# Performance work log

Measured on AMD Instinct MI355X. Metric: run time of the kernel, lower is better.

## Reference

```python
import jax, jax.numpy as jnp
import numpy as np

N_NODES = 100_000
N_EDGES = 3_200_000
WEIGHT_LIMIT = 5000.0
RIDGE = 1e-7


def _polynomial_basis(diff):
    # diff: [E, 2] -> [E, 5] basis (x, y, x*y, x^2, y^2)
    x = diff[:, 0]
    y = diff[:, 1]
    return jnp.stack([x, y, x * y, x * x, y * y], axis=-1)


def setup_inputs() -> dict:
    key = jax.random.key(0)
    k1, k2, k3 = jax.random.split(key, 3)
    pos = jax.random.normal(k1, (N_NODES, 2), dtype=jnp.float32)
    row = jax.random.randint(k2, (N_EDGES,), 0, N_NODES, dtype=jnp.int64)
    col = jax.random.randint(k3, (N_EDGES,), 0, N_NODES, dtype=jnp.int64)
    edge_index = jnp.stack([row, col], axis=0)
    return {"pos": pos, "edge_index": edge_index}


def reference(pos, edge_index):
    # With a dense random graph, 2-hop extension adds no edges, so the
    # augmented edge_index equals the original edge_index.
    row = edge_index[0]
    col = edge_index[1]
    n = pos.shape[0]

    # Edge displacement (detached in the original module).
    diff = jax.lax.stop_gradient(pos[col] - pos[row])  # [E, 2]
    H = _polynomial_basis(diff).astype(jnp.float32)    # [E, 5]

    # Per-edge outer products, scatter-accumulated per source node.
    M_edge = H[:, :, None] * H[:, None, :]                          # [E, 5, 5]
    M_node = jax.ops.segment_sum(M_edge, row, num_segments=n)      # [N, 5, 5]
    M_node = M_node + RIDGE * jnp.eye(5, dtype=jnp.float32)

    # Laplacian RHS: [0, 0, 0, 2, 2] per node (coefficients of x^2, y^2).
    L = jnp.zeros((n, 5), dtype=jnp.float32).at[:, 3:].set(2.0)

    # C = M^{-1} L (per-node 5x5 solve).
    C = jnp.linalg.solve(M_node, L[..., None])[..., 0]              # [N, 5]

    # Per-edge Laplacian weights.
    weights = jnp.sum(C[row] * H, axis=1)                           # [E]
    return jnp.clip(weights, -WEIGHT_LIMIT, WEIGHT_LIMIT)
```

## Files before the change

### kernel.cpp

```cpp
#include <hip/hip_runtime.h>
#include <math.h>

constexpr float WLIM = 5000.0f;
constexpr double RIDGE = 1e-7;

#define G 256
#define MAXNB 1024
#define BN 128
#define CAP 5120
#define EBUF_CAP 12544

__global__ __launch_bounds__(1024) void k_sort(const int* __restrict__ row,
                                               const int* __restrict__ col,
                                               int* __restrict__ table,
                                               unsigned int* __restrict__ sorted,
                                               int nE, int CE, int NB) {
    __shared__ int h[MAXNB];
    __shared__ int wt[16];
    __shared__ unsigned int ebuf[EBUF_CAP];
    const int g = blockIdx.x, tid = threadIdx.x;
    const int lane = tid & 63, wid = tid >> 6;
    const int s = g * CE;
    const int e_end = min(s + CE, nE);
    const int cnt = e_end - s;
    const bool vec = ((CE & 3) == 0);

    for (int i = tid; i < MAXNB; i += 1024) h[i] = 0;
    __syncthreads();
    if (vec) {
        const int4* r4p = (const int4*)(row + s);
        int nv = cnt >> 2;
        for (int i = tid; i < nv; i += 1024) {
            int4 r4 = r4p[i];
            atomicAdd(&h[r4.x >> 7], 1);
            atomicAdd(&h[r4.y >> 7], 1);
            atomicAdd(&h[r4.z >> 7], 1);
            atomicAdd(&h[r4.w >> 7], 1);
        }
        for (int i = (nv << 2) + tid; i < cnt; i += 1024)
            atomicAdd(&h[row[s + i] >> 7], 1);
    } else {
        for (int i = s + tid; i < e_end; i += 1024)
            atomicAdd(&h[row[i] >> 7], 1);
    }
    __syncthreads();
    int v = h[tid];
    int x = v;
    #pragma unroll
    for (int d = 1; d < 64; d <<= 1) {
        int u = __shfl_up(x, d);
        if (lane >= d) x += u;
    }
    if (lane == 63) wt[wid] = x;
    __syncthreads();
    if (tid < 16) {
        int w = wt[tid];
        int xx = w;
        #pragma unroll
        for (int d = 1; d < 16; d <<= 1) {
            int u = __shfl_up(xx, d);
            if (tid >= d) xx += u;
        }
        wt[tid] = xx - w;
    }
    __syncthreads();
    int excl = (x - v) + wt[wid];
    if (tid < NB) {
        table[(size_t)tid * G + g] = excl;
        h[tid] = excl;
    }
    if (tid == 0) table[(size_t)NB * G + g] = cnt;
    __syncthreads();
    if (vec) {
        const int4* r4p = (const int4*)(row + s);
        const int4* c4p = (const int4*)(col + s);
        int nv = cnt >> 2;
        for (int i = tid; i < nv; i += 1024) {
            int4 r4 = r4p[i];
            int4 c4 = c4p[i];
            int p;
            p = atomicAdd(&h[r4.x >> 7], 1); ebuf[p] = ((unsigned)(r4.x & 127) << 17) | (unsigned)c4.x;
            p = atomicAdd(&h[r4.y >> 7], 1); ebuf[p] = ((unsigned)(r4.y & 127) << 17) | (unsigned)c4.y;
            p = atomicAdd(&h[r4.z >> 7], 1); ebuf[p] = ((unsigned)(r4.z & 127) << 17) | (unsigned)c4.z;
            p = atomicAdd(&h[r4.w >> 7], 1); ebuf[p] = ((unsigned)(r4.w & 127) << 17) | (unsigned)c4.w;
        }
        for (int i = (nv << 2) + tid; i < cnt; i += 1024) {
            int r = row[s + i], c = col[s + i];
            int p = atomicAdd(&h[r >> 7], 1);
            ebuf[p] = ((unsigned)(r & 127) << 17) | (unsigned)c;
        }
    } else {
        for (int i = s + tid; i < e_end; i += 1024) {
            int r = row[i], c = col[i];
            int p = atomicAdd(&h[r >> 7], 1);
            ebuf[p] = ((unsigned)(r & 127) << 17) | (unsigned)c;
        }
    }
    __syncthreads();
    if (vec) {
        uint4* dst = (uint4*)(sorted + s);
        const uint4* src = (const uint4*)ebuf;
        int nv = cnt >> 2;
        for (int i = tid; i < nv; i += 1024) dst[i] = src[i];
        for (int i = (nv << 2) + tid; i < cnt; i += 1024) sorted[s + i] = ebuf[i];
    } else {
        for (int i = tid; i < cnt; i += 1024) sorted[s + i] = ebuf[i];
    }
}

__global__ __launch_bounds__(256) void k_node3(const float2* __restrict__ pos,
                                               const unsigned int* __restrict__ sorted,
                                               const int* __restrict__ table,
                                               float* __restrict__ rec,
                                               int nN, int CE, int NB) {
    __shared__ unsigned int ebuf[CAP];
    __shared__ int cnt[BN];
    __shared__ int off[BN + 1];
    __shared__ int cur[BN];
    __shared__ int goff0[G], glen[G];
    __shared__ int wt2[2];
    const int b = blockIdx.x, tid = threadIdx.x;

    int off0 = table[(size_t)b * G + tid];
    int off1 = table[(size_t)(b + 1) * G + tid];
    int len = off1 - off0;
    goff0[tid] = off0; glen[tid] = len;
    if (tid < BN) cnt[tid] = 0;
    __syncthreads();

    const int gbase = tid * CE + off0;
    for (int j = 0; j < len; ++j)
        atomicAdd(&cnt[sorted[gbase + j] >> 17], 1);
    __syncthreads();
    int sv = 0, sx = 0;
    if (tid < BN) {
        sv = cnt[tid];
        sx = sv;
        #pragma unroll
        for (int d = 1; d < 64; d <<= 1) {
            int u = __shfl_up(sx, d);
            if ((tid & 63) >= d) sx += u;
        }
        if ((tid & 63) == 63) wt2[tid >> 6] = sx;
    }
    __syncthreads();
    if (tid < BN) {
        int incl = sx + ((tid >> 6) ? wt2[0] : 0);
        off[tid] = incl - sv;
        cur[tid] = incl - sv;
        if (tid == BN - 1) off[BN] = incl;
    }
    __syncthreads();
    const int total = off[BN];

    const bool fits = (total <= CAP);
    if (fits) {
        for (int j = 0; j < len; ++j) {
            unsigned v = sorted[gbase + j];
            int p = atomicAdd(&cur[(int)(v >> 17)], 1);
            ebuf[p] = v & 0x1FFFFu;
        }
    }
    __syncthreads();

    const int node = tid >> 1;
    const int half = tid & 1;
    const int n = (b << 7) + node;
    float m[15];
    #pragma unroll
    for (int i = 0; i < 15; ++i) m[i] = 0.0f;
    float2 pr = make_float2(0.f, 0.f);
    if (n < nN) {
        pr = pos[n];
        if (fits) {
            int j0 = off[node], j1 = off[node + 1];
            for (int j = j0 + half; j < j1; j += 2) {
                float2 pc = pos[ebuf[j]];
                float x = pc.x - pr.x;
                float y = pc.y - pr.y;
                float xy = x * y, xx = x * x, yy = y * y;
                m[0]  += x * x;   m[1]  += x * y;   m[2]  += x * xy;  m[3]  += x * xx;  m[4]  += x * yy;
                m[5]  += y * y;   m[6]  += y * xy;  m[7]  += y * xx;  m[8]  += y * yy;
                m[9]  += xy * xy; m[10] += xy * xx; m[11] += xy * yy;
                m[12] += xx * xx; m[13] += xx * yy;
                m[14] += yy * yy;
            }
        } else {
            for (int g2 = half; g2 < G; g2 += 2) {
                int base2 = g2 * CE + goff0[g2];
                for (int j = 0; j < glen[g2]; ++j) {
                    unsigned v = sorted[base2 + j];
                    if ((int)(v >> 17) == node) {
                        float2 pc = pos[v & 0x1FFFFu];
                        float x = pc.x - pr.x;
                        float y = pc.y - pr.y;
                        float xy = x * y, xx = x * x, yy = y * y;
                        m[0]  += x * x;   m[1]  += x * y;   m[2]  += x * xy;  m[3]  += x * xx;  m[4]  += x * yy;
                        m[5]  += y * y;   m[6]  += y * xy;  m[7]  += y * xx;  m[8]  += y * yy;
                        m[9]  += xy * xy; m[10] += xy * xx; m[11] += xy * yy;
                        m[12] += xx * xx; m[13] += xx * yy;
                        m[14] += yy * yy;
                    }
                }
            }
        }
    }
    #pragma unroll
    for (int i = 0; i < 15; ++i) m[i] += __shfl_xor(m[i], 1);

    if (half == 0 && n < nN) {
        double A[5][5];
        {
            int idx = 0;
            #pragma unroll
            for (int i = 0; i < 5; ++i) {
                #pragma unroll
                for (int j = i; j < 5; ++j) {
                    double vv = (double)m[idx++];
                    A[i][j] = vv;
                    A[j][i] = vv;
                }
            }
        }
        #pragma unroll
        for (int i = 0; i < 5; ++i) A[i][i] += RIDGE;

        #pragma unroll
        for (int k = 0; k < 5; ++k) {
            double d = A[k][k];
            d = sqrt(fmax(d, 1e-300));
            A[k][k] = d;
            double inv = 1.0 / d;
            #pragma unroll
            for (int i = k + 1; i < 5; ++i) A[i][k] *= inv;
            #pragma unroll
            for (int j = k + 1; j < 5; ++j) {
                #pragma unroll
                for (int i = j; i < 5; ++i) A[i][j] -= A[i][k] * A[j][k];
            }
        }
        double bb[5] = {0.0, 0.0, 0.0, 2.0, 2.0};
        double y[5];
        #pragma unroll
        for (int i = 0; i < 5; ++i) {
            double sv2 = bb[i];
            #pragma unroll
            for (int k = 0; k < 5; ++k) {
                if (k < i) sv2 -= A[i][k] * y[k];
            }
            y[i] = sv2 / A[i][i];
        }
        double xs[5];
        #pragma unroll
        for (int ii = 4; ii >= 0; --ii) {
            double sv2 = y[ii];
            #pragma unroll
            for (int k = 0; k < 5; ++k) {
                if (k > ii) sv2 -= A[k][ii] * xs[k];
            }
            xs[ii] = sv2 / A[ii][ii];
        }
        float4* rb = (float4*)(rec + (size_t)n * 8);
        rb[0] = make_float4((float)xs[0], (float)xs[1], (float)xs[2], (float)xs[3]);
        rb[1] = make_float4((float)xs[4], pr.x, pr.y, 0.0f);
    }
}

__global__ __launch_bounds__(256) void k_weights(const float2* __restrict__ pos,
                                                 const int* __restrict__ row,
                                                 const int* __restrict__ col,
                                                 const float* __restrict__ rec,
                                                 float* __restrict__ out,
                                                 int nE) {
    int e = blockIdx.x * blockDim.x + threadIdx.x;
    if (e >= nE) return;
    int r = __builtin_nontemporal_load(row + e);
    int c = __builtin_nontemporal_load(col + e);
    const float4* rb = (const float4*)(rec + (size_t)r * 8);
    float4 q0 = rb[0];
    float4 q1 = rb[1];
    float2 pc = pos[c];
    float x = pc.x - q1.y;
    float y = pc.y - q1.z;
    float w = q0.x * x + q0.y * y + q0.z * (x * y) + q0.w * (x * x) + q1.x * (y * y);
    w = fminf(fmaxf(w, -WLIM), WLIM);
    __builtin_nontemporal_store(w, out + e);
}

extern "C" void kernel_launch(void* const* d_in, const int* in_sizes, int n_in,
                              void* d_out, int out_size, void* d_ws, size_t ws_size,
                              hipStream_t stream) {
    const float2* pos = (const float2*)d_in[0];
    const int* ei = (const int*)d_in[1];
    const int nN = in_sizes[0] / 2;
    const int nE = in_sizes[1] / 2;
    const int* row = ei;
    const int* col = ei + nE;

    const int NB = (nN + BN - 1) >> 7;
    const int CE = (nE + G - 1) / G;

    int* table = (int*)d_ws;
    size_t roff = (((size_t)(NB + 1) * G) + 3) & ~(size_t)3;
    float* rec = (float*)((int*)d_ws + roff);

    unsigned int* sorted = (unsigned int*)d_out;
    float* out = (float*)d_out;

    k_sort<<<G, 1024, 0, stream>>>(row, col, table, sorted, nE, CE, NB);
    k_node3<<<NB, 256, 0, stream>>>(pos, sorted, table, rec, nN, CE, NB);
    k_weights<<<(nE + 255) / 256, 256, 0, stream>>>(pos, row, col, rec, out, nE);
}
```

Measured before the change: 85.12 us.

## Split edge bucketing into more smaller blocks and process two chunks per thread

The bucketing kernel now uses 512 blocks of 512 threads, each holding half the edge chunk in shared memory. Each thread now handles two histogram bins, and the chunk size is padded to a multiple of four so the vector path always applies. The node kernel reads two group chunks per thread, interleaved to expose more memory parallelism. The weights kernel moves to 1024-thread blocks. The intent is more parallelism and occupancy in the sort stage. The cost is a larger offset table and more serial work per thread in the node kernel.

```diff
diff --git a/kernel.cpp b/kernel.cpp
--- a/kernel.cpp
+++ b/kernel.cpp
@@ -4,47 +4,45 @@
 constexpr float WLIM = 5000.0f;
 constexpr double RIDGE = 1e-7;
 
-#define G 256
+#define G 512
+#define SBT 512
 #define MAXNB 1024
 #define BN 128
 #define CAP 5120
-#define EBUF_CAP 12544
-
-__global__ __launch_bounds__(1024) void k_sort(const int* __restrict__ row,
-                                               const int* __restrict__ col,
-                                               int* __restrict__ table,
-                                               unsigned int* __restrict__ sorted,
-                                               int nE, int CE, int NB) {
+#define EBUF_CAP 6272
+
+__global__ __launch_bounds__(SBT) void k_sort(const int* __restrict__ row,
+                                              const int* __restrict__ col,
+                                              int* __restrict__ table,
+                                              unsigned int* __restrict__ sorted,
+                                              int nE, int CE, int NB) {
     __shared__ int h[MAXNB];
-    __shared__ int wt[16];
+    __shared__ int wt[SBT / 64];
     __shared__ unsigned int ebuf[EBUF_CAP];
     const int g = blockIdx.x, tid = threadIdx.x;
     const int lane = tid & 63, wid = tid >> 6;
     const int s = g * CE;
     const int e_end = min(s + CE, nE);
-    const int cnt = e_end - s;
-    const bool vec = ((CE & 3) == 0);
-
-    for (int i = tid; i < MAXNB; i += 1024) h[i] = 0;
-    __syncthreads();
-    if (vec) {
+    const int cnt = max(0, e_end - s);
+
+    for (int i = tid; i < MAXNB; i += SBT) h[i] = 0;
+    __syncthreads();
+    {
         const int4* r4p = (const int4*)(row + s);
         int nv = cnt >> 2;
-        for (int i = tid; i < nv; i += 1024) {
+        for (int i = tid; i < nv; i += SBT) {
             int4 r4 = r4p[i];
             atomicAdd(&h[r4.x >> 7], 1);
             atomicAdd(&h[r4.y >> 7], 1);
             atomicAdd(&h[r4.z >> 7], 1);
             atomicAdd(&h[r4.w >> 7], 1);
         }
-        for (int i = (nv << 2) + tid; i < cnt; i += 1024)
+        for (int i = (nv << 2) + tid; i < cnt; i += SBT)
             atomicAdd(&h[row[s + i] >> 7], 1);
-    } else {
-        for (int i = s + tid; i < e_end; i += 1024)
-            atomicAdd(&h[row[i] >> 7], 1);
-    }
-    __syncthreads();
-    int v = h[tid];
+    }
+    __syncthreads();
+    int v0 = h[2 * tid], v1 = h[2 * tid + 1];
+    int v = v0 + v1;
     int x = v;
     #pragma unroll
     for (int d = 1; d < 64; d <<= 1) {
@@ -53,29 +51,30 @@
     }
     if (lane == 63) wt[wid] = x;
     __syncthreads();
-    if (tid < 16) {
+    if (tid < SBT / 64) {
         int w = wt[tid];
         int xx = w;
         #pragma unroll
-        for (int d = 1; d < 16; d <<= 1) {
+        for (int d = 1; d < SBT / 64; d <<= 1) {
             int u = __shfl_up(xx, d);
             if (tid >= d) xx += u;
         }
         wt[tid] = xx - w;
     }
     __syncthreads();
-    int excl = (x - v) + wt[wid];
-    if (tid < NB) {
-        table[(size_t)tid * G + g] = excl;
-        h[tid] = excl;
-    }
+    int base = (x - v) + wt[wid];
+    int e0 = base, e1 = base + v0;
+    if (2 * tid < NB)     table[(size_t)(2 * tid) * G + g] = e0;
+    if (2 * tid + 1 < NB) table[(size_t)(2 * tid + 1) * G + g] = e1;
     if (tid == 0) table[(size_t)NB * G + g] = cnt;
-    __syncthreads();
-    if (vec) {
+    h[2 * tid] = e0;
+    h[2 * tid + 1] = e1;
+    __syncthreads();
+    {
         const int4* r4p = (const int4*)(row + s);
         const int4* c4p = (const int4*)(col + s);
         int nv = cnt >> 2;
-        for (int i = tid; i < nv; i += 1024) {
+        for (int i = tid; i < nv; i += SBT) {
             int4 r4 = r4p[i];
             int4 c4 = c4p[i];
             int p;
@@ -84,27 +83,19 @@
             p = atomicAdd(&h[r4.z >> 7], 1); ebuf[p] = ((unsigned)(r4.z & 127) << 17) | (unsigned)c4.z;
             p = atomicAdd(&h[r4.w >> 7], 1); ebuf[p] = ((unsigned)(r4.w & 127) << 17) | (unsigned)c4.w;
         }
-        for (int i = (nv << 2) + tid; i < cnt; i += 1024) {
+        for (int i = (nv << 2) + tid; i < cnt; i += SBT) {
             int r = row[s + i], c = col[s + i];
             int p = atomicAdd(&h[r >> 7], 1);
             ebuf[p] = ((unsigned)(r & 127) << 17) | (unsigned)c;
         }
-    } else {
-        for (int i = s + tid; i < e_end; i += 1024) {
-            int r = row[i], c = col[i];
-            int p = atomicAdd(&h[r >> 7], 1);
-            ebuf[p] = ((unsigned)(r & 127) << 17) | (unsigned)c;
-        }
-    }
-    __syncthreads();
-    if (vec) {
+    }
+    __syncthreads();
+    {
         uint4* dst = (uint4*)(sorted + s);
         const uint4* src = (const uint4*)ebuf;
         int nv = cnt >> 2;
-        for (int i = tid; i < nv; i += 1024) dst[i] = src[i];
-        for (int i = (nv << 2) + tid; i < cnt; i += 1024) sorted[s + i] = ebuf[i];
-    } else {
-        for (int i = tid; i < cnt; i += 1024) sorted[s + i] = ebuf[i];
+        for (int i = tid; i < nv; i += SBT) dst[i] = src[i];
+        for (int i = (nv << 2) + tid; i < cnt; i += SBT) sorted[s + i] = ebuf[i];
     }
 }
 
@@ -120,17 +111,33 @@
     __shared__ int goff0[G], glen[G];
     __shared__ int wt2[2];
     const int b = blockIdx.x, tid = threadIdx.x;
-
-    int off0 = table[(size_t)b * G + tid];
-    int off1 = table[(size_t)(b + 1) * G + tid];
-    int len = off1 - off0;
-    goff0[tid] = off0; glen[tid] = len;
+    const int tB = tid + 256;
+
+    int offA0 = table[(size_t)b * G + tid];
+    int offA1 = table[(size_t)(b + 1) * G + tid];
+    int offB0 = table[(size_t)b * G + tB];
+    int offB1 = table[(size_t)(b + 1) * G + tB];
+    int lenA = offA1 - offA0;
+    int lenB = offB1 - offB0;
+    goff0[tid] = offA0; glen[tid] = lenA;
+    goff0[tB] = offB0;  glen[tB] = lenB;
     if (tid < BN) cnt[tid] = 0;
     __syncthreads();
 
-    const int gbase = tid * CE + off0;
-    for (int j = 0; j < len; ++j)
-        atomicAdd(&cnt[sorted[gbase + j] >> 17], 1);
+    const int gbaseA = tid * CE + offA0;
+    const int gbaseB = tB * CE + offB0;
+    {
+        int j = 0;
+        int lmin = min(lenA, lenB);
+        for (; j < lmin; ++j) {
+            unsigned va = sorted[gbaseA + j];
+            unsigned vb = sorted[gbaseB + j];
+            atomicAdd(&cnt[va >> 17], 1);
+            atomicAdd(&cnt[vb >> 17], 1);
+        }
+        for (; j < lenA; ++j) atomicAdd(&cnt[sorted[gbaseA + j] >> 17], 1);
+        for (; j < lenB; ++j) atomicAdd(&cnt[sorted[gbaseB + j] >> 17], 1);
+    }
     __syncthreads();
     int sv = 0, sx = 0;
     if (tid < BN) {
@@ -155,10 +162,25 @@
 
     const bool fits = (total <= CAP);
     if (fits) {
-        for (int j = 0; j < len; ++j) {
-            unsigned v = sorted[gbase + j];
-            int p = atomicAdd(&cur[(int)(v >> 17)], 1);
-            ebuf[p] = v & 0x1FFFFu;
+        int j = 0;
+        int lmin = min(lenA, lenB);
+        for (; j < lmin; ++j) {
+            unsigned va = sorted[gbaseA + j];
+            unsigned vb = sorted[gbaseB + j];
+            int pa = atomicAdd(&cur[(int)(va >> 17)], 1);
+            ebuf[pa] = va & 0x1FFFFu;
+            int pb = atomicAdd(&cur[(int)(vb >> 17)], 1);
+            ebuf[pb] = vb & 0x1FFFFu;
+        }
+        for (; j < lenA; ++j) {
+            unsigned va = sorted[gbaseA + j];
+            int pa = atomicAdd(&cur[(int)(va >> 17)], 1);
+            ebuf[pa] = va & 0x1FFFFu;
+        }
+        for (; j < lenB; ++j) {
+            unsigned vb = sorted[gbaseB + j];
+            int pb = atomicAdd(&cur[(int)(vb >> 17)], 1);
+            ebuf[pb] = vb & 0x1FFFFu;
         }
     }
     __syncthreads();
@@ -266,12 +288,12 @@
     }
 }
 
-__global__ __launch_bounds__(256) void k_weights(const float2* __restrict__ pos,
-                                                 const int* __restrict__ row,
-                                                 const int* __restrict__ col,
-                                                 const float* __restrict__ rec,
-                                                 float* __restrict__ out,
-                                                 int nE) {
+__global__ __launch_bounds__(1024) void k_weights(const float2* __restrict__ pos,
+                                                  const int* __restrict__ row,
+                                                  const int* __restrict__ col,
+                                                  const float* __restrict__ rec,
+                                                  float* __restrict__ out,
+                                                  int nE) {
     int e = blockIdx.x * blockDim.x + threadIdx.x;
     if (e >= nE) return;
     int r = __builtin_nontemporal_load(row + e);
@@ -298,7 +320,7 @@
     const int* col = ei + nE;
 
     const int NB = (nN + BN - 1) >> 7;
-    const int CE = (nE + G - 1) / G;
+    const int CE = (((nE + G - 1) / G) + 3) & ~3;
 
     int* table = (int*)d_ws;
     size_t roff = (((size_t)(NB + 1) * G) + 3) & ~(size_t)3;
@@ -307,7 +329,7 @@
     unsigned int* sorted = (unsigned int*)d_out;
     float* out = (float*)d_out;
 
-    k_sort<<<G, 1024, 0, stream>>>(row, col, table, sorted, nE, CE, NB);
+    k_sort<<<G, SBT, 0, stream>>>(row, col, table, sorted, nE, CE, NB);
     k_node3<<<NB, 256, 0, stream>>>(pos, sorted, table, rec, nN, CE, NB);
-    k_weights<<<(nE + 255) / 256, 256, 0, stream>>>(pos, row, col, rec, out, nE);
+    k_weights<<<(nE + 1023) / 1024, 1024, 0, stream>>>(pos, row, col, rec, out, nE);
 }
```

Result: slower. 114.4 us (+34.4%).

## Compute edge weights in sorted order inside node kernel, then unsort via posmap

Applied to the files above, without the earlier changes.

The separate per-edge weights kernel is removed. Each node block now keeps its solved coefficients in shared memory and computes weights for its bucket-sorted edges, writing them in place over the sorted buffer. The sort kernel also records a 16-bit local position for every edge. A new unsort kernel uses that position to put the weights back in original edge order. This avoids re-reading row/col and gathering per-node records from global memory, but adds posmap traffic, an extra full pass over the edges, and a per-thread serial loop with poorly coalesced accesses in the node kernel.

```diff
diff --git a/kernel.cpp b/kernel.cpp
--- a/kernel.cpp
+++ b/kernel.cpp
@@ -14,6 +14,7 @@
                                                const int* __restrict__ col,
                                                int* __restrict__ table,
                                                unsigned int* __restrict__ sorted,
+                                               unsigned short* __restrict__ posmap,
                                                int nE, int CE, int NB) {
     __shared__ int h[MAXNB];
     __shared__ int wt[16];
@@ -74,26 +75,30 @@
     if (vec) {
         const int4* r4p = (const int4*)(row + s);
         const int4* c4p = (const int4*)(col + s);
+        ushort4* pm4 = (ushort4*)(posmap + s);
         int nv = cnt >> 2;
         for (int i = tid; i < nv; i += 1024) {
             int4 r4 = r4p[i];
             int4 c4 = c4p[i];
-            int p;
-            p = atomicAdd(&h[r4.x >> 7], 1); ebuf[p] = ((unsigned)(r4.x & 127) << 17) | (unsigned)c4.x;
-            p = atomicAdd(&h[r4.y >> 7], 1); ebuf[p] = ((unsigned)(r4.y & 127) << 17) | (unsigned)c4.y;
-            p = atomicAdd(&h[r4.z >> 7], 1); ebuf[p] = ((unsigned)(r4.z & 127) << 17) | (unsigned)c4.z;
-            p = atomicAdd(&h[r4.w >> 7], 1); ebuf[p] = ((unsigned)(r4.w & 127) << 17) | (unsigned)c4.w;
+            int p0 = atomicAdd(&h[r4.x >> 7], 1); ebuf[p0] = ((unsigned)(r4.x & 127) << 17) | (unsigned)c4.x;
+            int p1 = atomicAdd(&h[r4.y >> 7], 1); ebuf[p1] = ((unsigned)(r4.y & 127) << 17) | (unsigned)c4.y;
+            int p2 = atomicAdd(&h[r4.z >> 7], 1); ebuf[p2] = ((unsigned)(r4.z & 127) << 17) | (unsigned)c4.z;
+            int p3 = atomicAdd(&h[r4.w >> 7], 1); ebuf[p3] = ((unsigned)(r4.w & 127) << 17) | (unsigned)c4.w;
+            pm4[i] = make_ushort4((unsigned short)p0, (unsigned short)p1,
+                                  (unsigned short)p2, (unsigned short)p3);
         }
         for (int i = (nv << 2) + tid; i < cnt; i += 1024) {
             int r = row[s + i], c = col[s + i];
             int p = atomicAdd(&h[r >> 7], 1);
             ebuf[p] = ((unsigned)(r & 127) << 17) | (unsigned)c;
+            posmap[s + i] = (unsigned short)p;
         }
     } else {
-        for (int i = s + tid; i < e_end; i += 1024) {
-            int r = row[i], c = col[i];
+        for (int i = tid; i < cnt; i += 1024) {
+            int r = row[s + i], c = col[s + i];
             int p = atomicAdd(&h[r >> 7], 1);
             ebuf[p] = ((unsigned)(r & 127) << 17) | (unsigned)c;
+            posmap[s + i] = (unsigned short)p;
         }
     }
     __syncthreads();
@@ -109,9 +114,8 @@
 }
 
 __global__ __launch_bounds__(256) void k_node3(const float2* __restrict__ pos,
-                                               const unsigned int* __restrict__ sorted,
+                                               unsigned int* __restrict__ sorted,
                                                const int* __restrict__ table,
-                                               float* __restrict__ rec,
                                                int nN, int CE, int NB) {
     __shared__ unsigned int ebuf[CAP];
     __shared__ int cnt[BN];
@@ -119,6 +123,7 @@
     __shared__ int cur[BN];
     __shared__ int goff0[G], glen[G];
     __shared__ int wt2[2];
+    __shared__ float crec[BN * 8];
     const int b = blockIdx.x, tid = threadIdx.x;
 
     int off0 = table[(size_t)b * G + tid];
@@ -260,31 +265,59 @@
             }
             xs[ii] = sv2 / A[ii][ii];
         }
-        float4* rb = (float4*)(rec + (size_t)n * 8);
-        rb[0] = make_float4((float)xs[0], (float)xs[1], (float)xs[2], (float)xs[3]);
-        rb[1] = make_float4((float)xs[4], pr.x, pr.y, 0.0f);
+        float* cb = &crec[node * 8];
+        #pragma unroll
+        for (int i = 0; i < 5; ++i) cb[i] = (float)xs[i];
+        cb[5] = pr.x;
+        cb[6] = pr.y;
+    }
+    __syncthreads();
+
+    float* wout = (float*)sorted;
+    for (int j = 0; j < len; ++j) {
+        unsigned v = sorted[gbase + j];
+        int lr = (int)(v >> 17);
+        int c = (int)(v & 0x1FFFFu);
+        const float* cb = &crec[lr * 8];
+        float2 pc = pos[c];
+        float x = pc.x - cb[5];
+        float y = pc.y - cb[6];
+        float w = cb[0] * x + cb[1] * y + cb[2] * (x * y) + cb[3] * (x * x) + cb[4] * (y * y);
+        w = fminf(fmaxf(w, -WLIM), WLIM);
+        wout[gbase + j] = w;
     }
 }
 
-__global__ __launch_bounds__(256) void k_weights(const float2* __restrict__ pos,
-                                                 const int* __restrict__ row,
-                                                 const int* __restrict__ col,
-                                                 const float* __restrict__ rec,
-                                                 float* __restrict__ out,
-                                                 int nE) {
-    int e = blockIdx.x * blockDim.x + threadIdx.x;
-    if (e >= nE) return;
-    int r = __builtin_nontemporal_load(row + e);
-    int c = __builtin_nontemporal_load(col + e);
-    const float4* rb = (const float4*)(rec + (size_t)r * 8);
-    float4 q0 = rb[0];
-    float4 q1 = rb[1];
-    float2 pc = pos[c];
-    float x = pc.x - q1.y;
-    float y = pc.y - q1.z;
-    float w = q0.x * x + q0.y * y + q0.z * (x * y) + q0.w * (x * x) + q1.x * (y * y);
-    w = fminf(fmaxf(w, -WLIM), WLIM);
-    __builtin_nontemporal_store(w, out + e);
+__global__ __launch_bounds__(1024) void k_unsort(const float* __restrict__ wsorted,
+                                                 const unsigned short* __restrict__ posmap,
+                                                 float* __restrict__ out, int nE, int CE) {
+    __shared__ float wl[EBUF_CAP];
+    const int g = blockIdx.x, tid = threadIdx.x;
+    const int s = g * CE;
+    const int e_end = min(s + CE, nE);
+    const int cnt = e_end - s;
+    const bool vec = ((CE & 3) == 0);
+    if (vec) {
+        const uint4* src = (const uint4*)(wsorted + s);
+        uint4* dstl = (uint4*)wl;
+        int nv = cnt >> 2;
+        for (int i = tid; i < nv; i += 1024) dstl[i] = src[i];
+        for (int i = (nv << 2) + tid; i < cnt; i += 1024) wl[i] = wsorted[s + i];
+        __syncthreads();
+        const ushort4* pm4 = (const ushort4*)(posmap + s);
+        float4* out4 = (float4*)(out + s);
+        for (int i = tid; i < nv; i += 1024) {
+            ushort4 p4 = pm4[i];
+            float4 o;
+            o.x = wl[p4.x]; o.y = wl[p4.y]; o.z = wl[p4.z]; o.w = wl[p4.w];
+            out4[i] = o;
+        }
+        for (int i = (nv << 2) + tid; i < cnt; i += 1024) out[s + i] = wl[posmap[s + i]];
+    } else {
+        for (int i = tid; i < cnt; i += 1024) wl[i] = wsorted[s + i];
+        __syncthreads();
+        for (int i = tid; i < cnt; i += 1024) out[s + i] = wl[posmap[s + i]];
+    }
 }
 
 extern "C" void kernel_launch(void* const* d_in, const int* in_sizes, int n_in,
@@ -301,13 +334,13 @@
     const int CE = (nE + G - 1) / G;
 
     int* table = (int*)d_ws;
-    size_t roff = (((size_t)(NB + 1) * G) + 3) & ~(size_t)3;
-    float* rec = (float*)((int*)d_ws + roff);
+    size_t poff_ints = (((size_t)(NB + 1) * G) + 1) & ~(size_t)1;
+    unsigned short* posmap = (unsigned short*)((int*)d_ws + poff_ints);
 
     unsigned int* sorted = (unsigned int*)d_out;
     float* out = (float*)d_out;
 
-    k_sort<<<G, 1024, 0, stream>>>(row, col, table, sorted, nE, CE, NB);
-    k_node3<<<NB, 256, 0, stream>>>(pos, sorted, table, rec, nN, CE, NB);
-    k_weights<<<(nE + 255) / 256, 256, 0, stream>>>(pos, row, col, rec, out, nE);
+    k_sort<<<G, 1024, 0, stream>>>(row, col, table, sorted, posmap, nE, CE, NB);
+    k_node3<<<NB, 256, 0, stream>>>(pos, sorted, table, nN, CE, NB);
+    k_unsort<<<G, 1024, 0, stream>>>((const float*)sorted, posmap, out, nE, CE);
 }
```

Result: slower. 90.08 us (+5.8%).
